# Optimization experiments

Measured on AMD Instinct MI355X. Metric: run time of the kernel, lower is better.

The kernel has to match this reference:

```python
import jax, jax.numpy as jnp
import numpy as np

N_NODES = 100000
N_EDGES = 3200000
IN_CH = 128
HID_CH = 64
NEG_SLOPE = 0.2  # PyG GATConv default leaky_relu slope


def setup_inputs() -> dict:
    key = jax.random.key(0)
    k1, k2, k3, k4, k5, k6 = jax.random.split(key, 6)
    x = jax.random.normal(k1, (N_NODES, IN_CH), dtype=jnp.float32)
    edge_index = jax.random.randint(k2, (2, N_EDGES), 0, N_NODES, dtype=jnp.int64)
    # learned params of GATConv(in, hid, heads=1)
    W = jax.random.normal(k3, (IN_CH, HID_CH), dtype=jnp.float32) / np.sqrt(IN_CH)
    att_src = jax.random.normal(k4, (HID_CH,), dtype=jnp.float32) / np.sqrt(HID_CH)
    att_dst = jax.random.normal(k5, (HID_CH,), dtype=jnp.float32) / np.sqrt(HID_CH)
    bias = jax.random.normal(k6, (HID_CH,), dtype=jnp.float32) * 0.01
    return {"x": x, "edge_index": edge_index, "W": W, "att_src": att_src,
            "att_dst": att_dst, "bias": bias}


def reference(x, edge_index, W, att_src, att_dst, bias):
    N = x.shape[0]
    h = x @ W  # [N, H] linear transform
    # PyG GATConv default: add self loops
    loops = jnp.arange(N, dtype=edge_index.dtype)
    src = jnp.concatenate([edge_index[0], loops])  # [E+N]
    dst = jnp.concatenate([edge_index[1], loops])
    # per-node attention halves, then gather per-edge
    a_src = h @ att_src  # [N]
    a_dst = h @ att_dst  # [N]
    e = jax.nn.leaky_relu(a_src[src] + a_dst[dst], NEG_SLOPE)  # [E+N]
    # segment softmax over incoming edges of each destination node
    m = jax.ops.segment_max(e, dst, num_segments=N)
    e = jnp.exp(e - m[dst])
    s = jax.ops.segment_sum(e, dst, num_segments=N)
    alpha = e / s[dst]  # [E+N]
    # scatter-aggregate weighted source features
    out = jax.ops.segment_sum(h[src] * alpha[:, None], dst, num_segments=N) + bias
    return out, alpha[:, None]
```

## Files before the change

kernel.cpp:

```cpp
#include <hip/hip_runtime.h>
#include <hip/hip_bf16.h>

#define IN_CH 128
#define HID 64
#define NEG_SLOPE 0.2f
#define BSH 8
#define CAP 10240

typedef __attribute__((ext_vector_type(8))) short short8;
typedef __attribute__((ext_vector_type(4))) float floatx4;
typedef __attribute__((ext_vector_type(2))) float f32x2;

__device__ inline short bfr(float f) {
    unsigned u = __float_as_uint(f);
    u += 0x7fffu + ((u >> 16) & 1u);
    return (short)(u >> 16);
}

__global__ void k_prep(const float* __restrict__ W, short* __restrict__ wfrag,
                       int* __restrict__ g_cursor)
{
    if (blockIdx.x == 0) {
        g_cursor[threadIdx.x] = 0;
        g_cursor[threadIdx.x + 256] = 0;
    }
    int idx = blockIdx.x * 256 + threadIdx.x;
    if (idx >= 1024) return;
    int f = idx >> 6, l = idx & 63;
    int kt = f >> 2, nt = f & 3;
    int k0 = kt * 32 + (l >> 4) * 8;
    int n = nt * 16 + (l & 15);
#pragma unroll
    for (int j = 0; j < 8; ++j)
        wfrag[idx * 8 + j] = bfr(W[(k0 + j) * HID + n]);
}

__global__ __launch_bounds__(256) void k_gemm(
    const float* __restrict__ x, const short8* __restrict__ wfrag,
    const float* __restrict__ att_src, const float* __restrict__ att_dst,
    short* __restrict__ h, float* __restrict__ a_src,
    float* __restrict__ a_dst, int N)
{
    const int t = threadIdx.x;
    const int lane = t & 63;
    const int wv = t >> 6;
    const int l15 = lane & 15;
    const int quad = lane >> 4;

    short8 bf[16];
#pragma unroll
    for (int f = 0; f < 16; ++f) bf[f] = wfrag[f * 64 + lane];

    float as4[4], ad4[4];
#pragma unroll
    for (int nt = 0; nt < 4; ++nt) {
        as4[nt] = att_src[nt * 16 + l15];
        ad4[nt] = att_dst[nt * 16 + l15];
    }

    const int rowbase = blockIdx.x * 128 + wv * 32;

#pragma unroll
    for (int mt = 0; mt < 2; ++mt) {
        const int m0 = rowbase + mt * 16;
        const int rowa = m0 + l15;
        const int rowc = rowa < N ? rowa : N - 1;
        const float* xp = x + (size_t)rowc * IN_CH + quad * 8;

        short8 af[4];
#pragma unroll
        for (int kt = 0; kt < 4; ++kt) {
            float4 p0 = *(const float4*)(xp + kt * 32);
            float4 p1 = *(const float4*)(xp + kt * 32 + 4);
            short8 a;
            a[0] = bfr(p0.x); a[1] = bfr(p0.y); a[2] = bfr(p0.z); a[3] = bfr(p0.w);
            a[4] = bfr(p1.x); a[5] = bfr(p1.y); a[6] = bfr(p1.z); a[7] = bfr(p1.w);
            af[kt] = a;
        }

        floatx4 acc[4];
#pragma unroll
        for (int nt = 0; nt < 4; ++nt) acc[nt] = (floatx4){0.f, 0.f, 0.f, 0.f};
#pragma unroll
        for (int kt = 0; kt < 4; ++kt)
#pragma unroll
            for (int nt = 0; nt < 4; ++nt)
                acc[nt] = __builtin_amdgcn_mfma_f32_16x16x32_bf16(
                    af[kt], bf[kt * 4 + nt], acc[nt], 0, 0, 0);

#pragma unroll
        for (int r = 0; r < 4; ++r) {
            const int row = m0 + quad * 4 + r;
            const bool ok = row < N;
            if (ok) {
#pragma unroll
                for (int nt = 0; nt < 4; ++nt)
                    h[(size_t)row * HID + nt * 16 + l15] = bfr(acc[nt][r]);
            }
            float ps = acc[0][r] * as4[0] + acc[1][r] * as4[1] +
                       acc[2][r] * as4[2] + acc[3][r] * as4[3];
            float pd = acc[0][r] * ad4[0] + acc[1][r] * ad4[1] +
                       acc[2][r] * ad4[2] + acc[3][r] * ad4[3];
#pragma unroll
            for (int m2 = 1; m2 < 16; m2 <<= 1) {
                ps += __shfl_xor(ps, m2, 64);
                pd += __shfl_xor(pd, m2, 64);
            }
            if (ok && l15 == 0) { a_src[row] = ps; a_dst[row] = pd; }
        }
    }
}

__global__ __launch_bounds__(256) void k_binB(
    const int* __restrict__ ei, int* __restrict__ g_cursor,
    int* __restrict__ pairs, int E, int nb)
{
    __shared__ int hist[512];
    __shared__ int base[512];
    const int t = threadIdx.x;
    hist[t] = 0;
    hist[t + 256] = 0;
    __syncthreads();

    int s[16], d[16];
    const int4* s4 = (const int4*)ei;
    const int4* d4 = (const int4*)(ei + E);
    const int E4 = E >> 2;
    const int q0 = blockIdx.x * 1024;
#pragma unroll
    for (int i = 0; i < 4; ++i) {
        int q = q0 + i * 256 + t;
        int4 sv = make_int4(0, 0, 0, 0);
        int4 dv = make_int4(-1, -1, -1, -1);
        if (q < E4) { sv = s4[q]; dv = d4[q]; }
        s[4 * i + 0] = sv.x; s[4 * i + 1] = sv.y; s[4 * i + 2] = sv.z; s[4 * i + 3] = sv.w;
        d[4 * i + 0] = dv.x; d[4 * i + 1] = dv.y; d[4 * i + 2] = dv.z; d[4 * i + 3] = dv.w;
    }
#pragma unroll
    for (int i = 0; i < 16; ++i)
        if (d[i] >= 0) atomicAdd(&hist[d[i] >> BSH], 1);
    __syncthreads();

    if (t < nb) base[t] = atomicAdd(&g_cursor[t], hist[t]);
    if (t + 256 < nb) base[t + 256] = atomicAdd(&g_cursor[t + 256], hist[t + 256]);
    __syncthreads();
    hist[t] = 0;
    hist[t + 256] = 0;
    __syncthreads();

#pragma unroll
    for (int i = 0; i < 16; ++i) {
        if (d[i] < 0) continue;
        int b = d[i] >> BSH;
        int l = atomicAdd(&hist[b], 1);
        int pos = base[b] + l;
        if (pos < CAP)
            pairs[b * CAP + pos] = s[i] | ((d[i] & 255) << 17);
    }
}

__global__ __launch_bounds__(512) void k_binC(
    const int* __restrict__ pairs, const int* __restrict__ g_cursor,
    int* __restrict__ row_start, int* __restrict__ cnt,
    int* __restrict__ csr_src, int N, int nb)
{
    __shared__ int h0[256];
    __shared__ int hs[512];
    __shared__ int cur[256];
    __shared__ int sbase;
    const int t = threadIdx.x;
    const int b = blockIdx.x;
    const int d0 = b << BSH;
    const int m = g_cursor[b];
    const int* pb = pairs + b * CAP;

    int bv = (t < nb) ? g_cursor[t] : 0;
    hs[t] = bv;
    __syncthreads();
    for (int off = 1; off < 512; off <<= 1) {
        int u = (t >= off) ? hs[t - off] : 0;
        __syncthreads();
        hs[t] += u;
        __syncthreads();
    }
    if (t == b) sbase = hs[t] - bv;
    if (t < 256) h0[t] = 0;
    __syncthreads();
    const int basec = sbase;

    for (int i = t; i < m; i += 512)
        atomicAdd(&h0[pb[i] >> 17], 1);
    __syncthreads();

    if (t < 256) hs[t] = h0[t];
    __syncthreads();
    for (int off = 1; off < 256; off <<= 1) {
        int u = (t >= off && t < 256) ? hs[t - off] : 0;
        __syncthreads();
        if (t < 256) hs[t] += u;
        __syncthreads();
    }
    if (t < 256) {
        const int excl = hs[t] - h0[t];
        cur[t] = basec + excl;
        const int dd = d0 + t;
        if (dd < N) { row_start[dd] = basec + excl; cnt[dd] = h0[t]; }
    }
    __syncthreads();

    for (int i = t; i < m; i += 512) {
        int p = pb[i];
        int pos = atomicAdd(&cur[p >> 17], 1);
        csr_src[pos] = p & 0x1FFFF;
    }
}

__global__ __launch_bounds__(256) void k_agg(
    const __hip_bfloat16* __restrict__ h, const float* __restrict__ a_src,
    const float* __restrict__ a_dst, const float* __restrict__ bias,
    const int* __restrict__ row_start, const int* __restrict__ cnt,
    const int* __restrict__ csr_src,
    float* __restrict__ out, float2* __restrict__ adi, int N)
{
    __shared__ float red[4][2][576];

    const int wave = threadIdx.x >> 6;
    const int lane = threadIdx.x & 63;
    const int d0 = blockIdx.x * 8 + wave * 2;
    if (d0 >= N) return;
    const int d1 = d0 + 1;
    const bool has1 = d1 < N;

    const int q  = lane >> 3;
    const int i8 = lane & 7;

    const float2 ad2 = *(const float2*)(a_dst + d0);
    const float ad0 = ad2.x;
    const float ad1 = ad2.y;
    const int2 cn2 = *(const int2*)(cnt + d0);
    const int n0 = cn2.x;
    const int n1 = has1 ? cn2.y : 0;
    const int st0 = row_start[d0];
    const int en0 = st0 + n0;
    const int st1 = en0;
    const int en1 = st1 + n1;

    const uint4* h4 = (const uint4*)h;

    float ps0 = 0.f, ps1 = 0.f;
    f32x2 ac0[4], ac1[4];
#pragma unroll
    for (int c = 0; c < 4; ++c) {
        ac0[c] = (f32x2){0.f, 0.f};
        ac1[c] = (f32x2){0.f, 0.f};
    }

    const int nbt0 = (n0 + 63) >> 6;
    const int nbt1 = (n1 + 63) >> 6;
    const int nbm = nbt0 > nbt1 ? nbt0 : nbt1;

    int b0 = st0, b1 = st1;
    for (int it = 0; it < nbm; ++it, b0 += 64, b1 += 64) {
        int s0v = 0, s1v = 0;
        float e0 = 0.f, e1 = 0.f;
        const int idx0 = b0 + lane;
        if (it < nbt0 && idx0 < en0) {
            s0v = csr_src[idx0];
            float v = a_src[s0v] + ad0;
            v = v > 0.f ? v : NEG_SLOPE * v;
            e0 = __expf(v);
            ps0 += e0;
        }
        const int idx1 = b1 + lane;
        if (it < nbt1 && idx1 < en1) {
            s1v = csr_src[idx1];
            float v = a_src[s1v] + ad1;
            v = v > 0.f ? v : NEG_SLOPE * v;
            e1 = __expf(v);
            ps1 += e1;
        }
        const int m0 = (it < nbt0) ? min(64, en0 - b0) : 0;
        const int m1 = (it < nbt1) ? min(64, en1 - b1) : 0;
        const int mm = m0 > m1 ? m0 : m1;
#pragma unroll 4
        for (int j = 0; j < mm; j += 8) {
            const int jq = j + q;
            const int sj0 = __shfl(s0v, jq, 64);
            const float ej0 = __shfl(e0, jq, 64);
            const int sj1 = __shfl(s1v, jq, 64);
            const float ej1 = __shfl(e1, jq, 64);
            uint4 u0 = h4[(size_t)sj0 * 8 + i8];
            uint4 u1 = h4[(size_t)sj1 * 8 + i8];
            f32x2 ev0; ev0[0] = ej0; ev0[1] = ej0;
            f32x2 ev1; ev1[0] = ej1; ev1[1] = ej1;
            f32x2 c;
            c[0] = __uint_as_float(u0.x << 16);
            c[1] = __uint_as_float(u0.x & 0xffff0000u);
            ac0[0] = __builtin_elementwise_fma(ev0, c, ac0[0]);
            c[0] = __uint_as_float(u0.y << 16);
            c[1] = __uint_as_float(u0.y & 0xffff0000u);
            ac0[1] = __builtin_elementwise_fma(ev0, c, ac0[1]);
            c[0] = __uint_as_float(u0.z << 16);
            c[1] = __uint_as_float(u0.z & 0xffff0000u);
            ac0[2] = __builtin_elementwise_fma(ev0, c, ac0[2]);
            c[0] = __uint_as_float(u0.w << 16);
            c[1] = __uint_as_float(u0.w & 0xffff0000u);
            ac0[3] = __builtin_elementwise_fma(ev0, c, ac0[3]);
            c[0] = __uint_as_float(u1.x << 16);
            c[1] = __uint_as_float(u1.x & 0xffff0000u);
            ac1[0] = __builtin_elementwise_fma(ev1, c, ac1[0]);
            c[0] = __uint_as_float(u1.y << 16);
            c[1] = __uint_as_float(u1.y & 0xffff0000u);
            ac1[1] = __builtin_elementwise_fma(ev1, c, ac1[1]);
            c[0] = __uint_as_float(u1.z << 16);
            c[1] = __uint_as_float(u1.z & 0xffff0000u);
            ac1[2] = __builtin_elementwise_fma(ev1, c, ac1[2]);
            c[0] = __uint_as_float(u1.w << 16);
            c[1] = __uint_as_float(u1.w & 0xffff0000u);
            ac1[3] = __builtin_elementwise_fma(ev1, c, ac1[3]);
        }
    }

    float* r0 = &red[wave][0][0];
    float* r1 = &red[wave][1][0];
#pragma unroll
    for (int p = 0; p < 4; ++p) {
        r0[(i8 * 8 + 2 * p) * 9 + q]     = ac0[p][0];
        r0[(i8 * 8 + 2 * p + 1) * 9 + q] = ac0[p][1];
        r1[(i8 * 8 + 2 * p) * 9 + q]     = ac1[p][0];
        r1[(i8 * 8 + 2 * p + 1) * 9 + q] = ac1[p][1];
    }

#pragma unroll
    for (int m2 = 32; m2 > 0; m2 >>= 1) {
        ps0 += __shfl_xor(ps0, m2, 64);
        ps1 += __shfl_xor(ps1, m2, 64);
    }

    const float2 asd = *(const float2*)(a_src + d0);
    float vs0 = asd.x + ad0;
    vs0 = vs0 > 0.f ? vs0 : NEG_SLOPE * vs0;
    const float es0 = __expf(vs0);
    const float inv0 = 1.f / (ps0 + es0);
    float es1 = 0.f, inv1 = 0.f;
    if (has1) {
        float vs1 = asd.y + ad1;
        vs1 = vs1 > 0.f ? vs1 : NEG_SLOPE * vs1;
        es1 = __expf(vs1);
        inv1 = 1.f / (ps1 + es1);
    }
    if (lane == 0) {
        adi[d0] = make_float2(ad0, inv0);
        if (has1) adi[d1] = make_float2(ad1, inv1);
    }

    float s0 = 0.f, s1 = 0.f;
#pragma unroll
    for (int qq = 0; qq < 8; ++qq) {
        s0 += r0[lane * 9 + qq];
        s1 += r1[lane * 9 + qq];
    }

    const ushort* hu = (const ushort*)h;
    const float bi = bias[lane];
    float hs0 = __uint_as_float(((unsigned)hu[(size_t)d0 * HID + lane]) << 16);
    out[(size_t)d0 * HID + lane] = fmaf(es0, hs0, s0) * inv0 + bi;
    if (has1) {
        float hs1 = __uint_as_float(((unsigned)hu[(size_t)d1 * HID + lane]) << 16);
        out[(size_t)d1 * HID + lane] = fmaf(es1, hs1, s1) * inv1 + bi;
    }
}

__global__ void k_alpha(const int* __restrict__ ei,
                        const float* __restrict__ a_src,
                        const float2* __restrict__ adi,
                        float* __restrict__ out_alpha, int E, int N)
{
    int e = blockIdx.x * 256 + threadIdx.x;
    if (e >= E + N) return;
    int s, d;
    if (e < E) { s = ei[e]; d = ei[E + e]; }
    else       { s = e - E; d = s; }
    float2 av = adi[d];
    float v = a_src[s] + av.x;
    v = v > 0.f ? v : NEG_SLOPE * v;
    out_alpha[e] = __expf(v) * av.y;
}

extern "C" void kernel_launch(void* const* d_in, const int* in_sizes, int n_in,
                              void* d_out, int out_size, void* d_ws, size_t ws_size,
                              hipStream_t stream)
{
    (void)n_in; (void)out_size; (void)ws_size;
    const float* x       = (const float*)d_in[0];
    const int*   ei      = (const int*)d_in[1];
    const float* W       = (const float*)d_in[2];
    const float* att_src = (const float*)d_in[3];
    const float* att_dst = (const float*)d_in[4];
    const float* bias    = (const float*)d_in[5];

    const int N = in_sizes[0] / IN_CH;
    const int E = in_sizes[1] / 2;
    const int T = E + N;
    const int nb = (N + 255) >> BSH;

    __hip_bfloat16* h = (__hip_bfloat16*)d_ws;
    float* a_src_d = (float*)(h + (size_t)N * HID);
    float* a_dst_d = a_src_d + N;
    float2* adi    = (float2*)(a_dst_d + N);
    int* row_start = (int*)(adi + N);
    int* cnt       = row_start + N;
    int* g_cursor  = cnt + N;
    short* wfrag   = (short*)(g_cursor + 512);
    int* pairs     = (int*)(wfrag + 8192);
    int* csr_src   = pairs + (size_t)nb * CAP;

    float* out       = (float*)d_out;
    float* out_alpha = out + (size_t)N * HID;

    k_prep<<<4, 256, 0, stream>>>(W, wfrag, g_cursor);
    k_gemm<<<(N + 127) / 128, 256, 0, stream>>>(x, (const short8*)wfrag,
                                                att_src, att_dst,
                                                (short*)h, a_src_d, a_dst_d, N);
    k_binB<<<(E / 4 + 1023) / 1024, 256, 0, stream>>>(ei, g_cursor, pairs, E, nb);
    k_binC<<<nb, 512, 0, stream>>>(pairs, g_cursor,
                                   row_start, cnt, csr_src, N, nb);
    k_agg<<<(N + 7) / 8, 256, 0, stream>>>(h, a_src_d, a_dst_d, bias,
                                           row_start, cnt, csr_src,
                                           out, adi, N);
    k_alpha<<<(T + 255) / 256, 256, 0, stream>>>(ei, a_src_d, adi,
                                                 out_alpha, E, N);
}
```

Measured before the change: 268.5 us.

## Reuse first-pass atomic ranks in binning and vectorize alpha kernel

```diff
diff --git a/kernel.cpp b/kernel.cpp
--- a/kernel.cpp
+++ b/kernel.cpp
@@ -6,6 +6,7 @@
 #define NEG_SLOPE 0.2f
 #define BSH 8
 #define CAP 10240
+#define KPT 20
 
 typedef __attribute__((ext_vector_type(8))) short short8;
 typedef __attribute__((ext_vector_type(4))) float floatx4;
@@ -122,7 +123,7 @@
     hist[t + 256] = 0;
     __syncthreads();
 
-    int s[16], d[16];
+    int s[16], d[16], l[16];
     const int4* s4 = (const int4*)ei;
     const int4* d4 = (const int4*)(ei + E);
     const int E4 = E >> 2;
@@ -138,22 +139,18 @@
     }
 #pragma unroll
     for (int i = 0; i < 16; ++i)
-        if (d[i] >= 0) atomicAdd(&hist[d[i] >> BSH], 1);
+        if (d[i] >= 0) l[i] = atomicAdd(&hist[d[i] >> BSH], 1);
     __syncthreads();
 
     if (t < nb) base[t] = atomicAdd(&g_cursor[t], hist[t]);
     if (t + 256 < nb) base[t + 256] = atomicAdd(&g_cursor[t + 256], hist[t + 256]);
-    __syncthreads();
-    hist[t] = 0;
-    hist[t + 256] = 0;
     __syncthreads();
 
 #pragma unroll
     for (int i = 0; i < 16; ++i) {
         if (d[i] < 0) continue;
         int b = d[i] >> BSH;
-        int l = atomicAdd(&hist[b], 1);
-        int pos = base[b] + l;
+        int pos = base[b] + l[i];
         if (pos < CAP)
             pairs[b * CAP + pos] = s[i] | ((d[i] & 255) << 17);
     }
@@ -166,12 +163,12 @@
 {
     __shared__ int h0[256];
     __shared__ int hs[512];
-    __shared__ int cur[256];
+    __shared__ int exc[256];
     __shared__ int sbase;
     const int t = threadIdx.x;
     const int b = blockIdx.x;
-    const int d0 = b << BSH;
-    const int m = g_cursor[b];
+    int m = g_cursor[b];
+    if (m > CAP) m = CAP;
     const int* pb = pairs + b * CAP;
 
     int bv = (t < nb) ? g_cursor[t] : 0;
@@ -186,10 +183,16 @@
     if (t == b) sbase = hs[t] - bv;
     if (t < 256) h0[t] = 0;
     __syncthreads();
-    const int basec = sbase;
-
-    for (int i = t; i < m; i += 512)
-        atomicAdd(&h0[pb[i] >> 17], 1);
+
+    int p[KPT], l[KPT];
+#pragma unroll
+    for (int k = 0; k < KPT; ++k) {
+        const int i = t + k * 512;
+        if (i < m) {
+            p[k] = pb[i];
+            l[k] = atomicAdd(&h0[p[k] >> 17], 1);
+        }
+    }
     __syncthreads();
 
     if (t < 256) hs[t] = h0[t];
@@ -200,18 +203,22 @@
         if (t < 256) hs[t] += u;
         __syncthreads();
     }
+    const int basec = sbase;
     if (t < 256) {
-        const int excl = hs[t] - h0[t];
-        cur[t] = basec + excl;
-        const int dd = d0 + t;
-        if (dd < N) { row_start[dd] = basec + excl; cnt[dd] = h0[t]; }
-    }
-    __syncthreads();
-
-    for (int i = t; i < m; i += 512) {
-        int p = pb[i];
-        int pos = atomicAdd(&cur[p >> 17], 1);
-        csr_src[pos] = p & 0x1FFFF;
+        const int e0 = hs[t] - h0[t];
+        exc[t] = e0;
+        const int dd = (b << BSH) + t;
+        if (dd < N) { row_start[dd] = basec + e0; cnt[dd] = h0[t]; }
+    }
+    __syncthreads();
+
+#pragma unroll
+    for (int k = 0; k < KPT; ++k) {
+        const int i = t + k * 512;
+        if (i < m) {
+            const int dl = p[k] >> 17;
+            csr_src[basec + exc[dl] + l[k]] = p[k] & 0x1FFFF;
+        }
     }
 }
 
@@ -376,15 +383,46 @@
                         const float2* __restrict__ adi,
                         float* __restrict__ out_alpha, int E, int N)
 {
-    int e = blockIdx.x * 256 + threadIdx.x;
-    if (e >= E + N) return;
-    int s, d;
-    if (e < E) { s = ei[e]; d = ei[E + e]; }
-    else       { s = e - E; d = s; }
-    float2 av = adi[d];
-    float v = a_src[s] + av.x;
-    v = v > 0.f ? v : NEG_SLOPE * v;
-    out_alpha[e] = __expf(v) * av.y;
+    const int E4 = E >> 2;
+    const int i = blockIdx.x * 256 + threadIdx.x;
+    if (i < E4) {
+        const int4 sv = ((const int4*)ei)[i];
+        const int4 dv = ((const int4*)(ei + E))[i];
+        float4 o;
+        {
+            const float2 av = adi[dv.x];
+            float v = a_src[sv.x] + av.x;
+            v = v > 0.f ? v : NEG_SLOPE * v;
+            o.x = __expf(v) * av.y;
+        }
+        {
+            const float2 av = adi[dv.y];
+            float v = a_src[sv.y] + av.x;
+            v = v > 0.f ? v : NEG_SLOPE * v;
+            o.y = __expf(v) * av.y;
+        }
+        {
+            const float2 av = adi[dv.z];
+            float v = a_src[sv.z] + av.x;
+            v = v > 0.f ? v : NEG_SLOPE * v;
+            o.z = __expf(v) * av.y;
+        }
+        {
+            const float2 av = adi[dv.w];
+            float v = a_src[sv.w] + av.x;
+            v = v > 0.f ? v : NEG_SLOPE * v;
+            o.w = __expf(v) * av.y;
+        }
+        ((float4*)out_alpha)[i] = o;
+    } else {
+        const int j = i - E4;
+        if (j < N) {
+            const float2 av = adi[j];
+            float v = a_src[j] + av.x;
+            v = v > 0.f ? v : NEG_SLOPE * v;
+            out_alpha[E + j] = __expf(v) * av.y;
+        }
+    }
 }
 
 extern "C" void kernel_launch(void* const* d_in, const int* in_sizes, int n_in,
@@ -401,7 +439,6 @@
 
     const int N = in_sizes[0] / IN_CH;
     const int E = in_sizes[1] / 2;
-    const int T = E + N;
     const int nb = (N + 255) >> BSH;
 
     __hip_bfloat16* h = (__hip_bfloat16*)d_ws;
@@ -428,6 +465,6 @@
     k_agg<<<(N + 7) / 8, 256, 0, stream>>>(h, a_src_d, a_dst_d, bias,
                                            row_start, cnt, csr_src,
                                            out, adi, N);
-    k_alpha<<<(T + 255) / 256, 256, 0, stream>>>(ei, a_src_d, adi,
-                                                 out_alpha, E, N);
-}
+    k_alpha<<<((E >> 2) + N + 255) / 256, 256, 0, stream>>>(ei, a_src_d, adi,
+                                                            out_alpha, E, N);
+}
```

Result: no change. 272.9 us (+1.6%).
